# Kernel optimization log

Measured on AMD Instinct MI355X. Metric: run time of the kernel, lower is better.

## Reference

```python
import jax, jax.numpy as jnp
import numpy as np
import math

B, S, D, H = 2, 2048, 1024, 16
DK = D // H


def setup_inputs() -> dict:
    key = jax.random.key(0)
    ks = jax.random.split(key, 10)
    sc = 1.0 / math.sqrt(D)
    inp = {
        "Q_input": jax.random.normal(ks[0], (B, S, D), dtype=jnp.float32),
        "Wq_w": jax.random.normal(ks[1], (D, D), dtype=jnp.float32) * sc,
        "Wq_b": jnp.zeros((D,), dtype=jnp.float32),
        "Wk_w": jax.random.normal(ks[2], (D, D), dtype=jnp.float32) * sc,
        "Wk_b": jnp.zeros((D,), dtype=jnp.float32),
        "Wv_w": jax.random.normal(ks[3], (D, D), dtype=jnp.float32) * sc,
        "Wv_b": jnp.zeros((D,), dtype=jnp.float32),
        "Wo_w": jax.random.normal(ks[4], (D, D), dtype=jnp.float32) * sc,
        "Wo_b": jnp.zeros((D,), dtype=jnp.float32),
        # causal mask, broadcast over batch and heads: [1,1,S,S]
        "mask": jnp.tril(jnp.ones((S, S), dtype=jnp.int32))[None, None],
    }
    return inp


def reference(Q_input, Wq_w, Wq_b, Wk_w, Wk_b, Wv_w, Wv_b, Wo_w, Wo_b, mask):
    b, s, _ = Q_input.shape
    # linear projections (torch Linear: x @ W^T + b)
    Q = Q_input @ Wq_w.T + Wq_b
    K = Q_input @ Wk_w.T + Wk_b
    V = Q_input @ Wv_w.T + Wv_b
    # [b, h, s, dk]
    Q = Q.reshape(b, s, H, DK).transpose(0, 2, 1, 3)
    K = K.reshape(b, s, H, DK).transpose(0, 2, 1, 3)
    V = V.reshape(b, s, H, DK).transpose(0, 2, 1, 3)
    scores = jnp.einsum("bhqd,bhkd->bhqk", Q, K) / math.sqrt(DK)
    scores = jnp.where(mask == 0, jnp.float32(-1e9), scores)
    weights = jax.nn.softmax(scores, axis=-1)
    attn = jnp.einsum("bhqk,bhkd->bhqd", weights, V)
    attn = attn.transpose(0, 2, 1, 3).reshape(b, s, D)
    return attn @ Wo_w.T + Wo_b
```

## Files before the change

### kernel.cpp

```cpp
#include <hip/hip_runtime.h>
#include <hip/hip_bf16.h>
#include <cstdint>

typedef __attribute__((ext_vector_type(8))) short short8;
typedef __attribute__((ext_vector_type(4))) float f32x4;
typedef __attribute__((ext_vector_type(2))) unsigned int uint2v;
typedef unsigned short ushort_t;

#define S_LEN 2048
#define D_DIM 1024
#define NH 16
#define DK 64
#define BATCH 2
#define M_ROWS (BATCH * S_LEN)
#define BK 32

__device__ inline ushort_t f2bf(float f) {
    union { float f; uint32_t u; } v; v.f = f;
    uint32_t r = v.u + 0x7fffu + ((v.u >> 16) & 1u);
    return (ushort_t)(r >> 16);
}

__device__ __forceinline__ ushort_t bfc(float f) {
    __hip_bfloat16 h = __float2bfloat16(f);
    return __builtin_bit_cast(ushort_t, h);
}

__device__ __forceinline__ float bf2f(ushort_t u) {
    return __uint_as_float(((uint32_t)u) << 16);
}

__device__ __forceinline__ float fexp2(float x) {
#if __has_builtin(__builtin_amdgcn_exp2f)
    return __builtin_amdgcn_exp2f(x);
#else
    return exp2f(x);
#endif
}
__device__ __forceinline__ float frcp(float x) {
#if __has_builtin(__builtin_amdgcn_rcpf)
    return __builtin_amdgcn_rcpf(x);
#else
    return 1.0f / x;
#endif
}

__device__ __forceinline__ void glds16(const ushort_t* g, ushort_t* l) {
    __builtin_amdgcn_global_load_lds(
        (const __attribute__((address_space(1))) uint32_t*)g,
        (__attribute__((address_space(3))) uint32_t*)l,
        16, 0, 0);
}

#if __has_builtin(__builtin_amdgcn_permlane16_swap) && __has_builtin(__builtin_amdgcn_permlane32_swap)
#define HAS_PLSWAP 1
#else
#define HAS_PLSWAP 0
#endif

__device__ __forceinline__ float red_max4(float x) {
#if HAS_PLSWAP
    uint2v a = __builtin_amdgcn_permlane16_swap(__float_as_uint(x), __float_as_uint(x), false, false);
    float y = fmaxf(__uint_as_float(a.x), __uint_as_float(a.y));
    uint2v b = __builtin_amdgcn_permlane32_swap(__float_as_uint(y), __float_as_uint(y), false, false);
    return fmaxf(__uint_as_float(b.x), __uint_as_float(b.y));
#else
    x = fmaxf(x, __shfl_xor(x, 16));
    return fmaxf(x, __shfl_xor(x, 32));
#endif
}
__device__ __forceinline__ float red_sum4(float x) {
#if HAS_PLSWAP
    uint2v a = __builtin_amdgcn_permlane16_swap(__float_as_uint(x), __float_as_uint(x), false, false);
    float y = __uint_as_float(a.x) + __uint_as_float(a.y);
    uint2v b = __builtin_amdgcn_permlane32_swap(__float_as_uint(y), __float_as_uint(y), false, false);
    return __uint_as_float(b.x) + __uint_as_float(b.y);
#else
    x += __shfl_xor(x, 16);
    return x + __shfl_xor(x, 32);
#endif
}

__device__ __forceinline__ void route_p(const uint32_t wp[4][2], int ks, int lane, uint32_t F[4]) {
#if HAS_PLSWAP
    uint32_t U0 = wp[2 * ks][0],     U1 = wp[2 * ks][1];
    uint32_t V0 = wp[2 * ks + 1][0], V1 = wp[2 * ks + 1][1];
    uint2v t, pa0, pa1, pb0, pb1;
    t = __builtin_amdgcn_permlane32_swap(U0, U0, false, false);
    pa0 = __builtin_amdgcn_permlane16_swap(U0, t.y, false, false);
    t = __builtin_amdgcn_permlane32_swap(U1, U1, false, false);
    pa1 = __builtin_amdgcn_permlane16_swap(U1, t.y, false, false);
    t = __builtin_amdgcn_permlane32_swap(V0, V0, false, false);
    pb0 = __builtin_amdgcn_permlane16_swap(t.x, V0, false, false);
    t = __builtin_amdgcn_permlane32_swap(V1, V1, false, false);
    pb1 = __builtin_amdgcn_permlane16_swap(t.x, V1, false, false);
    bool lo = lane < 32;
    F[0] = lo ? pa0.x : pb0.x;
    F[1] = lo ? pa1.x : pb1.x;
    F[2] = lo ? pa0.y : pb0.y;
    F[3] = lo ? pa1.y : pb1.y;
#else
    int q = lane & 15, g = lane >> 4;
#pragma unroll
    for (int m = 0; m < 4; m++) {
        int src = 16 * (2 * (g & 1) + (m >> 1)) + q;
        uint32_t xa = (uint32_t)__shfl((int)wp[2 * ks][m & 1], src);
        uint32_t xb = (uint32_t)__shfl((int)wp[2 * ks + 1][m & 1], src);
        F[m] = (g < 2) ? xa : xb;
    }
#endif
}

__global__ void cvt_bf16(const float* __restrict__ in, ushort_t* __restrict__ out, int n4) {
    int i = blockIdx.x * blockDim.x + threadIdx.x;
    int stride = gridDim.x * blockDim.x;
    for (int idx = i; idx < n4; idx += stride) {
        float4 v = ((const float4*)in)[idx];
        ushort4 o;
        o.x = f2bf(v.x); o.y = f2bf(v.y); o.z = f2bf(v.z); o.w = f2bf(v.w);
        ((ushort4*)out)[idx] = o;
    }
}

__global__ void cvt_w3(const float* __restrict__ wq, const float* __restrict__ wk,
                       const float* __restrict__ wv, ushort_t* __restrict__ wqkv) {
    const int seg = (D_DIM * D_DIM) / 4;
    int i = blockIdx.x * blockDim.x + threadIdx.x;
    int stride = gridDim.x * blockDim.x;
    for (int idx = i; idx < 3 * seg; idx += stride) {
        int sel = idx >> 18;
        int id = idx & (seg - 1);
        const float* src = sel == 0 ? wq : (sel == 1 ? wk : wv);
        float4 v = ((const float4*)src)[id];
        ushort4 o;
        o.x = f2bf(v.x); o.y = f2bf(v.y); o.z = f2bf(v.z); o.w = f2bf(v.w);
        ((ushort4*)wqkv)[sel * seg + id] = o;
    }
}

template<int MODE, int BMt, int BNt>
__global__ __launch_bounds__(256) void gemm_bt(const ushort_t* __restrict__ A,
                                               const ushort_t* __restrict__ Bw,
                                               const float* __restrict__ b0,
                                               const float* __restrict__ b1,
                                               const float* __restrict__ b2,
                                               void* __restrict__ C0,
                                               void* __restrict__ C1,
                                               void* __restrict__ C2,
                                               int M, int N, int K) {
    constexpr int FM = BMt / 32, FN = BNt / 32;
    constexpr int ACH = BMt / 64, BCH = BNt / 64;
    __shared__ ushort_t As[BMt * BK];
    __shared__ ushort_t Bs[BNt * BK];
    int tid = threadIdx.x;
    int lane = tid & 63;
    int w = tid >> 6;
    int wr = w >> 1, wc = w & 1;
    int nwg = gridDim.x;
    int bx = (blockIdx.x & 7) * (nwg >> 3) + (blockIdx.x >> 3);
    int ntile = N / BNt;
    int m0 = (bx / ntile) * BMt;
    int n0 = (bx % ntile) * BNt;
    int lr = lane & 15;
    int lk = (lane >> 4) * 8;
    int srow = lane >> 2;
    int scol = (lane & 3) * 8;

    f32x4 acc[FM][FN] = {};

    for (int kt = 0; kt < K; kt += BK) {
        __syncthreads();
#pragma unroll
        for (int c = 0; c < ACH; c++)
            glds16(&A[(size_t)(m0 + w * (BMt / 4) + c * 16 + srow) * K + kt + scol],
                   &As[(w * (BMt / 4) + c * 16) * BK]);
#pragma unroll
        for (int c = 0; c < BCH; c++)
            glds16(&Bw[(size_t)(n0 + w * (BNt / 4) + c * 16 + srow) * K + kt + scol],
                   &Bs[(w * (BNt / 4) + c * 16) * BK]);
        __syncthreads();

        short8 af[FM], bf[FN];
#pragma unroll
        for (int f = 0; f < FM; f++)
            af[f] = *(const short8*)&As[(wr * (BMt / 2) + f * 16 + lr) * BK + lk];
#pragma unroll
        for (int f = 0; f < FN; f++)
            bf[f] = *(const short8*)&Bs[(wc * (BNt / 2) + f * 16 + lr) * BK + lk];
#pragma unroll
        for (int i = 0; i < FM; i++)
#pragma unroll
            for (int j = 0; j < FN; j++)
                acc[i][j] = __builtin_amdgcn_mfma_f32_16x16x32_bf16(af[i], bf[j], acc[i][j], 0, 0, 0);
    }

    int r0 = (lane >> 4) * 4;
#pragma unroll
    for (int j = 0; j < FN; j++) {
        int ncol = n0 + wc * (BNt / 2) + j * 16 + lr;
        if (MODE == 2) {
            float bv = b0[ncol];
#pragma unroll
            for (int i = 0; i < FM; i++) {
                int mbase = m0 + wr * (BMt / 2) + i * 16 + r0;
#pragma unroll
                for (int r = 0; r < 4; r++)
                    ((float*)C0)[(size_t)(mbase + r) * N + ncol] = acc[i][j][r] + bv;
            }
        } else {
            int sel = n0 >> 10;
            const float* bp = sel == 0 ? b0 : (sel == 1 ? b1 : b2);
            int nc = ncol & 1023;
            float bv = bp[nc];
            int hh = nc >> 6, dk = nc & 63;
            ushort_t* Co = (ushort_t*)(sel == 0 ? C0 : (sel == 1 ? C1 : C2));
#pragma unroll
            for (int i = 0; i < FM; i++) {
                int mbase = m0 + wr * (BMt / 2) + i * 16 + r0;
                int bb = mbase >> 11, ss = mbase & 2047;
                if (sel == 2) {
                    ushort4 pk;
                    pk.x = f2bf(acc[i][j][0] + bv);
                    pk.y = f2bf(acc[i][j][1] + bv);
                    pk.z = f2bf(acc[i][j][2] + bv);
                    pk.w = f2bf(acc[i][j][3] + bv);
                    size_t idx = ((size_t)(bb * NH + hh) * DK + dk) * S_LEN + ss;
                    *(ushort4*)&Co[idx] = pk;
                } else {
#pragma unroll
                    for (int r = 0; r < 4; r++) {
                        size_t idx = ((size_t)(bb * NH + hh) * S_LEN + (ss + r)) * DK + dk;
                        Co[idx] = f2bf(acc[i][j][r] + bv);
                    }
                }
            }
        }
    }
}

#define CSC 0.1803368801f

__device__ const unsigned char JTAB[48] = {
    30,31,31,15,28,29,29,30,
    25,24,13,28,27,27,26,14,
    25,26,12,22,23,23,24,11,
    19,19,18,10,22,21,21,20,
    20, 9,16,17,17,18, 8,16,
     0, 1, 2, 3, 4, 5, 6, 7};
__device__ const unsigned char KTAB[48] = {
     0, 0, 1, 9, 0, 0, 1, 1,
     0, 0, 9, 1, 1, 0, 0, 9,
     1, 1, 9, 0, 0, 1, 1, 9,
     1, 0, 0, 9, 1, 1, 0, 0,
     1, 9, 0, 0, 1, 1, 9, 1,
     9, 9, 9, 9, 9, 9, 9, 9};

__global__ __launch_bounds__(256) void attn_fwd(const ushort_t* __restrict__ Q,
                                                const ushort_t* __restrict__ K,
                                                const ushort_t* __restrict__ Vt,
                                                ushort_t* __restrict__ Oa,
                                                float2* __restrict__ ml,
                                                float* __restrict__ Pd) {
    __shared__ ushort_t Ks[2][64 * 64];
    __shared__ ushort_t Vs[2][64 * 64];

    int tid = threadIdx.x;
    int lane = tid & 63;
    int w = tid >> 6;
    int bh = blockIdx.x;
    int yy = blockIdx.y;
    int j = JTAB[yy];
    int kk = KTAB[yy];
    int nt = j + 1;
    int half = (nt + 1) >> 1;
    int t0 = (kk == 1) ? half : 0;
    int t1 = (kk == 0) ? half : nt;
    int cnt = t1 - t0;
    int off = yy % cnt;
    size_t base = (size_t)bh * S_LEN * DK;
    int q0 = j * 64;

    int lr = lane & 15;
    int lk = (lane >> 4) * 8;
    int g16 = (lane >> 4) * 16;
    int r0 = (lane >> 4) * 4;
    int wq = w * 16 + lr;

    auto swz = [](int row, int cb) { return (row * 128 + (cb ^ ((row & 7) << 4))) >> 1; };

    short8 qf0 = *(const short8*)&Q[base + (size_t)(q0 + wq) * DK + lk];
    short8 qf1 = *(const short8*)&Q[base + (size_t)(q0 + wq) * DK + 32 + lk];

    f32x4 o[4] = {};
    float mrowL = -1e30f, lrow = 0.f;

    int sr = tid >> 3;
    int scb = (tid & 7) * 16;
    int sce = (tid & 7) * 8;

    {
        int tf = t0 + off;
        *(uint4*)&Ks[0][swz(sr, scb)]      = *(const uint4*)&K [base + (size_t)(tf * 64 + sr) * DK + sce];
        *(uint4*)&Ks[0][swz(sr + 32, scb)] = *(const uint4*)&K [base + (size_t)(tf * 64 + sr + 32) * DK + sce];
        *(uint4*)&Vs[0][swz(sr, scb)]      = *(const uint4*)&Vt[base + (size_t)sr * S_LEN + tf * 64 + sce];
        *(uint4*)&Vs[0][swz(sr + 32, scb)] = *(const uint4*)&Vt[base + (size_t)(sr + 32) * S_LEN + tf * 64 + sce];
    }
    __syncthreads();

    int cur = 0;
    for (int s = 0; s < cnt; ++s) {
        int to = s + off; if (to >= cnt) to -= cnt;
        int t = t0 + to;
        bool last = (s == cnt - 1);
        bool diag = (t == j);
        uint4 kr0, kr1, vr0, vr1;
        if (!last) {
            int tno = s + 1 + off; if (tno >= cnt) tno -= cnt;
            int tn = t0 + tno;
            kr0 = *(const uint4*)&K [base + (size_t)(tn * 64 + sr) * DK + sce];
            kr1 = *(const uint4*)&K [base + (size_t)(tn * 64 + sr + 32) * DK + sce];
            vr0 = *(const uint4*)&Vt[base + (size_t)sr * S_LEN + tn * 64 + sce];
            vr1 = *(const uint4*)&Vt[base + (size_t)(sr + 32) * S_LEN + tn * 64 + sce];
        }

        f32x4 st[4] = {};
        __builtin_amdgcn_s_setprio(1);
#pragma unroll
        for (int n = 0; n < 4; n++) {
            if (!diag || n <= w) {
                short8 kf0 = *(const short8*)&Ks[cur][swz(n * 16 + lr, g16)];
                short8 kf1 = *(const short8*)&Ks[cur][swz(n * 16 + lr, 64 + g16)];
                st[n] = __builtin_amdgcn_mfma_f32_16x16x32_bf16(kf0, qf0, st[n], 0, 0, 0);
                st[n] = __builtin_amdgcn_mfma_f32_16x16x32_bf16(kf1, qf1, st[n], 0, 0, 0);
            }
        }
        __builtin_amdgcn_s_setprio(0);

        if (diag) {
#pragma unroll
            for (int n = 0; n < 4; n++)
#pragma unroll
                for (int i = 0; i < 4; i++)
                    if (16 * n + r0 + i > wq) st[n][i] = -1e30f;
        }

        float m0 = fmaxf(fmaxf(fmaxf(st[0][0], st[0][1]), st[0][2]), st[0][3]);
        float m1 = fmaxf(fmaxf(fmaxf(st[1][0], st[1][1]), st[1][2]), st[1][3]);
        float m2 = fmaxf(fmaxf(fmaxf(st[2][0], st[2][1]), st[2][2]), st[2][3]);
        float m3 = fmaxf(fmaxf(fmaxf(st[3][0], st[3][1]), st[3][2]), st[3][3]);
        float mx = fmaxf(fmaxf(fmaxf(m0, m1), m2), m3);
        float mxL = red_max4(mx) * CSC;

        bool skip = __all(mxL <= mrowL + 8.0f);
        float corr = 1.0f;
        float mnewL = mrowL;
        if (!skip) {
            mnewL = fmaxf(mrowL, mxL);
            corr = fexp2(mrowL - mnewL);
            mrowL = mnewL;
        }

        float psum = 0.f;
        uint32_t wp[4][2];
#pragma unroll
        for (int n = 0; n < 4; n++) {
#pragma unroll
            for (int i = 0; i < 4; i++) {
                float p = fexp2(fmaf(st[n][i], CSC, -mnewL));
                st[n][i] = p;
                psum += p;
            }
            wp[n][0] = (uint32_t)bfc(st[n][0]) | ((uint32_t)bfc(st[n][1]) << 16);
            wp[n][1] = (uint32_t)bfc(st[n][2]) | ((uint32_t)bfc(st[n][3]) << 16);
        }
        psum = red_sum4(psum);

        if (skip) {
            lrow += psum;
        } else {
            lrow = lrow * corr + psum;
            float cb[4];
#pragma unroll
            for (int i = 0; i < 4; i++) cb[i] = __shfl(corr, r0 + i);
#pragma unroll
            for (int d = 0; d < 4; d++)
#pragma unroll
                for (int i = 0; i < 4; i++) o[d][i] *= cb[i];
        }

#pragma unroll
        for (int ks = 0; ks < 2; ks++) {
            if (diag && 32 * ks > w * 16 + 15) continue;
            uint32_t F[4];
            route_p(wp, ks, lane, F);
            union { uint32_t u[4]; short8 s; } pu;
            pu.u[0] = F[0]; pu.u[1] = F[1]; pu.u[2] = F[2]; pu.u[3] = F[3];
            short8 pf = pu.s;
            __builtin_amdgcn_s_setprio(1);
#pragma unroll
            for (int d = 0; d < 4; d++) {
                short8 vf = *(const short8*)&Vs[cur][swz(d * 16 + lr, ks * 64 + g16)];
                o[d] = __builtin_amdgcn_mfma_f32_16x16x32_bf16(pf, vf, o[d], 0, 0, 0);
            }
            __builtin_amdgcn_s_setprio(0);
        }

        if (!last) {
            *(uint4*)&Ks[cur ^ 1][swz(sr, scb)]      = kr0;
            *(uint4*)&Ks[cur ^ 1][swz(sr + 32, scb)] = kr1;
            *(uint4*)&Vs[cur ^ 1][swz(sr, scb)]      = vr0;
            *(uint4*)&Vs[cur ^ 1][swz(sr + 32, scb)] = vr1;
        }
        __syncthreads();
        cur ^= 1;
    }

    int b = bh >> 4, h = bh & 15;
    if (kk == 9) {
        float lb[4];
#pragma unroll
        for (int i = 0; i < 4; i++) lb[i] = frcp(__shfl(lrow, r0 + i));
#pragma unroll
        for (int d = 0; d < 4; d++)
#pragma unroll
            for (int i = 0; i < 4; i++) {
                int qq = q0 + w * 16 + r0 + i;
                int dk = d * 16 + lr;
                size_t idx = ((size_t)(b * S_LEN + qq)) * D_DIM + h * DK + dk;
                Oa[idx] = bfc(o[d][i] * lb[i]);
            }
    } else {
        int jj = j - 16;
        if (kk == 0) {
#pragma unroll
            for (int d = 0; d < 4; d++)
#pragma unroll
                for (int i = 0; i < 4; i++) {
                    int qq = q0 + w * 16 + r0 + i;
                    int dk = d * 16 + lr;
                    size_t idx = ((size_t)(b * S_LEN + qq)) * D_DIM + h * DK + dk;
                    Oa[idx] = bfc(o[d][i]);
                }
        } else {
#pragma unroll
            for (int d = 0; d < 4; d++)
#pragma unroll
                for (int i = 0; i < 4; i++) {
                    int rloc = w * 16 + r0 + i;
                    Pd[((size_t)(bh * 16 + jj) * 64 + rloc) * 64 + d * 16 + lr] = o[d][i];
                }
        }
        if (lane < 16) {
            int row = w * 16 + lane;
            ml[(size_t)kk * 32768 + (bh * 16 + jj) * 64 + row] = make_float2(mrowL, lrow);
        }
    }
}

__global__ __launch_bounds__(256) void attn_merge(const float2* __restrict__ ml,
                                                  const float* __restrict__ Pd,
                                                  ushort_t* __restrict__ Oa) {
    int bh = blockIdx.x;
    int jj = blockIdx.y;
    int tid = threadIdx.x;
    int r = tid >> 2;
    int q = (tid & 3) * 16;
    int b = bh >> 4, h = bh & 15;
    int row = (jj + 16) * 64 + r;
    float2 a = ml[(bh * 16 + jj) * 64 + r];
    float2 c = ml[32768 + (bh * 16 + jj) * 64 + r];
    float M = fmaxf(a.x, c.x);
    float w0 = fexp2(a.x - M), w1 = fexp2(c.x - M);
    float rc = frcp(a.y * w0 + c.y * w1);
    size_t ob = ((size_t)(b * S_LEN + row)) * D_DIM + h * DK + q;
    const float* p1 = &Pd[((size_t)(bh * 16 + jj) * 64 + r) * 64 + q];
#pragma unroll
    for (int i = 0; i < 4; i++) {
        ushort4 o0 = *(const ushort4*)&Oa[ob + i * 4];
        float4 o1 = *(const float4*)&p1[i * 4];
        ushort4 res;
        res.x = bfc((bf2f(o0.x) * w0 + o1.x * w1) * rc);
        res.y = bfc((bf2f(o0.y) * w0 + o1.y * w1) * rc);
        res.z = bfc((bf2f(o0.z) * w0 + o1.z * w1) * rc);
        res.w = bfc((bf2f(o0.w) * w0 + o1.w * w1) * rc);
        *(ushort4*)&Oa[ob + i * 4] = res;
    }
}

extern "C" void kernel_launch(void* const* d_in, const int* in_sizes, int n_in,
                              void* d_out, int out_size, void* d_ws, size_t ws_size,
                              hipStream_t stream) {
    const float* X  = (const float*)d_in[0];
    const float* Wq = (const float*)d_in[1];
    const float* bq = (const float*)d_in[2];
    const float* Wk = (const float*)d_in[3];
    const float* bk = (const float*)d_in[4];
    const float* Wv = (const float*)d_in[5];
    const float* bv = (const float*)d_in[6];
    const float* Wo = (const float*)d_in[7];
    const float* bo = (const float*)d_in[8];
    float* out = (float*)d_out;

    char* ws = (char*)d_ws;
    ushort_t* Xb    = (ushort_t*)ws;
    ushort_t* Wqkvb = (ushort_t*)(ws + (8u  << 20));
    float2*   mlbuf = (float2*)(ws + (8u  << 20));
    ushort_t* Qb    = (ushort_t*)(ws + (14u << 20));
    ushort_t* Kb    = (ushort_t*)(ws + (22u << 20));
    ushort_t* Vtb   = (ushort_t*)(ws + (30u << 20));
    ushort_t* Wob   = Wqkvb;
    ushort_t* Ab    = Xb;
    float*    Pd    = out;

    const int M = M_ROWS;
    int nX4 = (M * D_DIM) / 4;
    int nW4 = (D_DIM * D_DIM) / 4;

    cvt_bf16<<<2048, 256, 0, stream>>>(X, Xb, nX4);
    cvt_w3<<<2048, 256, 0, stream>>>(Wq, Wk, Wv, Wqkvb);

    gemm_bt<3, 128, 128><<<dim3((M / 128) * (3072 / 128)), 256, 0, stream>>>(
        Xb, Wqkvb, bq, bk, bv, Qb, Kb, Vtb, M, 3072, D_DIM);

    dim3 agrid(BATCH * NH, 48);
    attn_fwd<<<agrid, 256, 0, stream>>>(Qb, Kb, Vtb, Ab, mlbuf, Pd);

    attn_merge<<<dim3(BATCH * NH, 16), 256, 0, stream>>>(mlbuf, Pd, Ab);

    cvt_bf16<<<2048, 256, 0, stream>>>(Wo, Wob, nW4);

    gemm_bt<2, 64, 128><<<dim3((M / 64) * (D_DIM / 128)), 256, 0, stream>>>(
        Ab, Wob, bo, bo, bo, out, out, out, M, D_DIM, D_DIM);
}
```

Measured before the change: 126.3 us.

## Load K and V fragments directly from global memory, dropping LDS staging

Removes the double-buffered shared-memory staging of K and V tiles and the per-iteration barrier in the attention kernel. Each wave now reads its MFMA operand fragments straight from global memory, with V fragments fetched at the start of the iteration. This removes LDS traffic and block-level synchronisation. In exchange, every wave re-reads the same K/V tile from global/L2, and the explicit prefetch of the next tile is lost.

```diff
diff --git a/kernel.cpp b/kernel.cpp
--- a/kernel.cpp
+++ b/kernel.cpp
@@ -261,9 +261,6 @@
                                                 ushort_t* __restrict__ Oa,
                                                 float2* __restrict__ ml,
                                                 float* __restrict__ Pd) {
-    __shared__ ushort_t Ks[2][64 * 64];
-    __shared__ ushort_t Vs[2][64 * 64];
-
     int tid = threadIdx.x;
     int lane = tid & 63;
     int w = tid >> 6;
@@ -282,45 +279,30 @@
 
     int lr = lane & 15;
     int lk = (lane >> 4) * 8;
-    int g16 = (lane >> 4) * 16;
     int r0 = (lane >> 4) * 4;
     int wq = w * 16 + lr;
 
-    auto swz = [](int row, int cb) { return (row * 128 + (cb ^ ((row & 7) << 4))) >> 1; };
-
     short8 qf0 = *(const short8*)&Q[base + (size_t)(q0 + wq) * DK + lk];
     short8 qf1 = *(const short8*)&Q[base + (size_t)(q0 + wq) * DK + 32 + lk];
 
     f32x4 o[4] = {};
     float mrowL = -1e30f, lrow = 0.f;
 
-    int sr = tid >> 3;
-    int scb = (tid & 7) * 16;
-    int sce = (tid & 7) * 8;
-
-    {
-        int tf = t0 + off;
-        *(uint4*)&Ks[0][swz(sr, scb)]      = *(const uint4*)&K [base + (size_t)(tf * 64 + sr) * DK + sce];
-        *(uint4*)&Ks[0][swz(sr + 32, scb)] = *(const uint4*)&K [base + (size_t)(tf * 64 + sr + 32) * DK + sce];
-        *(uint4*)&Vs[0][swz(sr, scb)]      = *(const uint4*)&Vt[base + (size_t)sr * S_LEN + tf * 64 + sce];
-        *(uint4*)&Vs[0][swz(sr + 32, scb)] = *(const uint4*)&Vt[base + (size_t)(sr + 32) * S_LEN + tf * 64 + sce];
-    }
-    __syncthreads();
-
-    int cur = 0;
     for (int s = 0; s < cnt; ++s) {
         int to = s + off; if (to >= cnt) to -= cnt;
         int t = t0 + to;
-        bool last = (s == cnt - 1);
         bool diag = (t == j);
-        uint4 kr0, kr1, vr0, vr1;
-        if (!last) {
-            int tno = s + 1 + off; if (tno >= cnt) tno -= cnt;
-            int tn = t0 + tno;
-            kr0 = *(const uint4*)&K [base + (size_t)(tn * 64 + sr) * DK + sce];
-            kr1 = *(const uint4*)&K [base + (size_t)(tn * 64 + sr + 32) * DK + sce];
-            vr0 = *(const uint4*)&Vt[base + (size_t)sr * S_LEN + tn * 64 + sce];
-            vr1 = *(const uint4*)&Vt[base + (size_t)(sr + 32) * S_LEN + tn * 64 + sce];
+        const ushort_t* Kt = K  + base + (size_t)(t * 64) * DK;
+        const ushort_t* Vp = Vt + base + t * 64;
+
+        short8 vf[4][2];
+#pragma unroll
+        for (int ks = 0; ks < 2; ks++) {
+            if (!diag || 32 * ks <= w * 16 + 15) {
+#pragma unroll
+                for (int d = 0; d < 4; d++)
+                    vf[d][ks] = *(const short8*)&Vp[(size_t)(d * 16 + lr) * S_LEN + ks * 32 + lk];
+            }
         }
 
         f32x4 st[4] = {};
@@ -328,8 +310,8 @@
 #pragma unroll
         for (int n = 0; n < 4; n++) {
             if (!diag || n <= w) {
-                short8 kf0 = *(const short8*)&Ks[cur][swz(n * 16 + lr, g16)];
-                short8 kf1 = *(const short8*)&Ks[cur][swz(n * 16 + lr, 64 + g16)];
+                short8 kf0 = *(const short8*)&Kt[(n * 16 + lr) * DK + lk];
+                short8 kf1 = *(const short8*)&Kt[(n * 16 + lr) * DK + 32 + lk];
                 st[n] = __builtin_amdgcn_mfma_f32_16x16x32_bf16(kf0, qf0, st[n], 0, 0, 0);
                 st[n] = __builtin_amdgcn_mfma_f32_16x16x32_bf16(kf1, qf1, st[n], 0, 0, 0);
             }
@@ -398,21 +380,10 @@
             short8 pf = pu.s;
             __builtin_amdgcn_s_setprio(1);
 #pragma unroll
-            for (int d = 0; d < 4; d++) {
-                short8 vf = *(const short8*)&Vs[cur][swz(d * 16 + lr, ks * 64 + g16)];
-                o[d] = __builtin_amdgcn_mfma_f32_16x16x32_bf16(pf, vf, o[d], 0, 0, 0);
-            }
+            for (int d = 0; d < 4; d++)
+                o[d] = __builtin_amdgcn_mfma_f32_16x16x32_bf16(pf, vf[d][ks], o[d], 0, 0, 0);
             __builtin_amdgcn_s_setprio(0);
         }
-
-        if (!last) {
-            *(uint4*)&Ks[cur ^ 1][swz(sr, scb)]      = kr0;
-            *(uint4*)&Ks[cur ^ 1][swz(sr + 32, scb)] = kr1;
-            *(uint4*)&Vs[cur ^ 1][swz(sr, scb)]      = vr0;
-            *(uint4*)&Vs[cur ^ 1][swz(sr + 32, scb)] = vr1;
-        }
-        __syncthreads();
-        cur ^= 1;
     }
 
     int b = bh >> 4, h = bh & 15;
```

New measurement: 215.7 us. 70.8% more time.
